# Optimization experiments

Measured on AMD Instinct MI355X. Metric: run time of the kernel, lower is better.

## Reference

```python
import jax, jax.numpy as jnp
import numpy as np

B, C, H, W = 16, 512, 32, 32
HW = H * W  # == input_features == output_features for shapes to be consistent


def setup_inputs() -> dict:
    key = jax.random.key(0)
    k1, k2, k3 = jax.random.split(key, 3)
    node1 = jax.random.normal(k1, (B, C, H, W), dtype=jnp.float32)
    node2 = jax.random.normal(k2, (B, C, H, W), dtype=jnp.float32)
    # nn.Linear(input_features, output_features, bias=False).weight: [out, in]
    W_c = jax.random.normal(k3, (HW, HW), dtype=jnp.float32) * (1.0 / np.sqrt(HW))
    return {"node1": node1, "node2": node2, "W_c": W_c}


def reference(node1, node2, W_c):
    b, c, h, w = node1.shape
    hw = h * w
    n1 = node1.reshape(b, c, hw)  # [B, C, HW]
    n2 = node2.reshape(b, c, hw)  # [B, C, HW]
    # x = W_c(n1): Linear applies y = x @ W^T  -> [B, C, HW_out]
    x = jnp.einsum('bch,oh->bco', n1, W_c)
    # e = bmm(x.permute(0,2,1), n2): [B, HW_out, C] @ [B, C, HW] -> [B, HW_out, HW]
    e = jnp.einsum('bco,bch->boh', x, n2)
    a = jax.nn.softmax(e, axis=-1)  # softmax over last dim (HW of node2)
    # m = bmm(n2, a): [B, C, HW] @ [B, HW, HW] -> [B, C, HW]
    m = jnp.einsum('bck,bkj->bcj', n2, a)
    return m
```

## Files before the change

kernel.cpp:

```cpp
#include <hip/hip_runtime.h>
#include <math.h>


typedef _Float16 f16;
typedef _Float16 f16x8 __attribute__((ext_vector_type(8)));
typedef _Float16 f16x4 __attribute__((ext_vector_type(4)));
typedef float f32x4 __attribute__((ext_vector_type(4)));

#define WG_BARRIER() asm volatile("s_waitcnt lgkmcnt(0)\ns_barrier" ::: "memory")

__global__ __launch_bounds__(256) void prep(const float* __restrict__ n1,
                                            const float* __restrict__ Wc,
                                            const float* __restrict__ n2,
                                            f16* __restrict__ n1f, f16* __restrict__ Wf,
                                            f16* __restrict__ n2f, f16* __restrict__ n2t) {
    const int bid = blockIdx.x, tid = threadIdx.x;
    if (bid < 4608) {
        const float* s = (bid < 4096) ? n1 : Wc;
        f16* d = (bid < 4096) ? n1f : Wf;
        const size_t i = ((size_t)(bid < 4096 ? bid : bid - 4096) * 256 + tid) * 8;
        f32x4 a = *(const f32x4*)(s + i);
        f32x4 b = *(const f32x4*)(s + i + 4);
        f16x8 o;
        o[0] = (f16)a[0]; o[1] = (f16)a[1]; o[2] = (f16)a[2]; o[3] = (f16)a[3];
        o[4] = (f16)b[0]; o[5] = (f16)b[1]; o[6] = (f16)b[2]; o[7] = (f16)b[3];
        *(f16x8*)(d + i) = o;
        return;
    }
    const int id = bid - 4608;
    const int b = id >> 7;
    const int ry = (id & 127) >> 4;
    const int cx = id & 15;
    const float* S = n2 + (size_t)b * 512 * 1024;
    f16* Dn = n2f + (size_t)b * 512 * 1024;
    f16* Dt = n2t + (size_t)b * 1024 * 512;
    __shared__ f16 Ts[64 * 72];
    const int r0 = ry * 64, c0 = cx * 64;
    const int rr = tid >> 3, cc8 = (tid & 7) * 8;
#pragma unroll
    for (int h = 0; h < 2; ++h) {
        const int row = r0 + rr + 32 * h;
        const float* s = S + (size_t)row * 1024 + c0 + cc8;
        f32x4 a = *(const f32x4*)s, bq = *(const f32x4*)(s + 4);
        f16x8 o;
        o[0] = (f16)a[0]; o[1] = (f16)a[1]; o[2] = (f16)a[2]; o[3] = (f16)a[3];
        o[4] = (f16)bq[0]; o[5] = (f16)bq[1]; o[6] = (f16)bq[2]; o[7] = (f16)bq[3];
        *(f16x8*)&Ts[(rr + 32 * h) * 72 + cc8] = o;
        *(f16x8*)(Dn + (size_t)row * 1024 + c0 + cc8) = o;
    }
    __syncthreads();
    const int j = tid >> 2, k16 = (tid & 3) * 16;
    f16* d = Dt + (size_t)(c0 + j) * 512 + r0 + k16;
    f16x8 o0, o1;
#pragma unroll
    for (int i = 0; i < 8; ++i) {
        o0[i] = Ts[(k16 + i) * 72 + j];
        o1[i] = Ts[(k16 + 8 + i) * 72 + j];
    }
    *(f16x8*)d = o0;
    *(f16x8*)(d + 8) = o1;
}

__global__ __launch_bounds__(256) void softmax_stats(const f16* __restrict__ E,
                                                     float* __restrict__ Mg,
                                                     float* __restrict__ Si) {
    const int wave = threadIdx.x >> 6, lane = threadIdx.x & 63;
    const int row = blockIdx.x * 4 + wave;
    const f16* p = E + (size_t)row * 1024 + lane * 16;
    f16x8 a = *(const f16x8*)p, b = *(const f16x8*)(p + 8);
    float v[16];
#pragma unroll
    for (int i = 0; i < 8; ++i) { v[i] = (float)a[i]; v[i + 8] = (float)b[i]; }
    float m = v[0];
#pragma unroll
    for (int i = 1; i < 16; ++i) m = fmaxf(m, v[i]);
#pragma unroll
    for (int off = 1; off < 64; off <<= 1) m = fmaxf(m, __shfl_xor(m, off, 64));
    float s = 0.f;
#pragma unroll
    for (int i = 0; i < 16; ++i) s += __expf(v[i] - m);
#pragma unroll
    for (int off = 1; off < 64; off <<= 1) s += __shfl_xor(s, off, 64);
    if (lane == 0) { Mg[row] = m; Si[row] = 1.0f / s; }
}

__global__ __launch_bounds__(256) void tr_scale(const f16* __restrict__ S,
                                                const float* __restrict__ Mg,
                                                const float* __restrict__ Si,
                                                f16* __restrict__ D) {
    const int b = blockIdx.z;
    S += (size_t)b * 1024 * 1024;
    D += (size_t)b * 1024 * 1024;
    __shared__ f16 Ts[64 * 72];
    const int r0 = blockIdx.y * 64, c0 = blockIdx.x * 64;
    const int tid = threadIdx.x;
    const int rr = tid >> 3, cc8 = (tid & 7) * 8;
#pragma unroll
    for (int h = 0; h < 2; ++h) {
        const int row = r0 + rr + 32 * h;
        const float mg = Mg[b * 1024 + row];
        const float si = Si[b * 1024 + row];
        f16x8 v = *(const f16x8*)(S + (size_t)row * 1024 + c0 + cc8);
        f16x8 o;
#pragma unroll
        for (int i = 0; i < 8; ++i) o[i] = (f16)(__expf((float)v[i] - mg) * si);
        *(f16x8*)&Ts[(rr + 32 * h) * 72 + cc8] = o;
    }
    __syncthreads();
    const int j = tid >> 2, k16 = (tid & 3) * 16;
    f16* d = D + (size_t)(c0 + j) * 1024 + r0 + k16;
    f16x8 o0, o1;
#pragma unroll
    for (int i = 0; i < 8; ++i) {
        o0[i] = Ts[(k16 + i) * 72 + j];
        o1[i] = Ts[(k16 + 8 + i) * 72 + j];
    }
    *(f16x8*)d = o0;
    *(f16x8*)(d + 8) = o1;
}

#define GEMM_CORE(NS)                                                                   \
    f16x8 ra = *(const f16x8*)gAp, rb = *(const f16x8*)gBp;                             \
    *(f16x8*)wA0 = ra; *(f16x8*)wB0 = rb;                                               \
    ra = *(const f16x8*)(gAp + 64); rb = *(const f16x8*)(gBp + 64);                     \
    WG_BARRIER();                                                                       \
    f32x4 acc[4][2] = {};                                                               \
_Pragma("unroll")                                                                       \
    for (int kb = 0; kb < (NS); ++kb) {                                                 \
        const f16* Ac = (const f16*)(SM + (kb & 1) * 8192);                             \
        const f16* Bc = (const f16*)(SM + 16384 + (kb & 1) * 8192);                     \
        f16x8 fa[4], fb[2];                                                             \
_Pragma("unroll")                                                                       \
        for (int u = 0; u < 4; ++u)                                                     \
            fa[u] = *(const f16x8*)&Ac[(wm + u * 16 + col) * 32 + quad * 8];            \
_Pragma("unroll")                                                                       \
        for (int v = 0; v < 2; ++v)                                                     \
            fb[v] = *(const f16x8*)&Bc[(wn + v * 16 + col) * 32 + quad * 8];            \
_Pragma("unroll")                                                                       \
        for (int u = 0; u < 4; ++u)                                                     \
_Pragma("unroll")                                                                       \
            for (int v = 0; v < 2; ++v)                                                 \
                acc[u][v] = __builtin_amdgcn_mfma_f32_16x16x32_f16(fa[u], fb[v],        \
                                                                   acc[u][v], 0, 0, 0);\
        if (kb + 1 < (NS)) {                                                            \
            char* dA = SM + ((kb + 1) & 1) * 8192 + off;                                \
            char* dB = SM + 16384 + ((kb + 1) & 1) * 8192 + off;                        \
            *(f16x8*)dA = ra;                                                           \
            *(f16x8*)dB = rb;                                                           \
            if (kb + 2 < (NS)) {                                                        \
                ra = *(const f16x8*)(gAp + (size_t)(kb + 2) * 64);                      \
                rb = *(const f16x8*)(gBp + (size_t)(kb + 2) * 64);                      \
            }                                                                           \
            WG_BARRIER();                                                               \
        }                                                                               \
    }

__global__ __launch_bounds__(512) void gemm1_nt_xt(const f16* __restrict__ A,
                                                   const f16* __restrict__ Bw,
                                                   f16* __restrict__ Xt) {
    const int M = 512, K = 1024;
    const int id = blockIdx.x;
    const int xcd = id & 7, loc = id >> 3;
    const int b = xcd * 2 + (loc >> 5);
    const int m0 = ((loc >> 3) & 3) * 128;
    const int n0 = (loc & 7) * 128;
    A += (size_t)b * M * K;
    Xt += (size_t)b * 1024 * M;
    __shared__ __attribute__((aligned(16))) char SM[34816];
    const int tid = threadIdx.x, lane = tid & 63, wave = tid >> 6;
    const int col = lane & 15, quad = lane >> 4;
    const int wm = (wave & 1) * 64, wn = (wave >> 1) * 32;
    const int off = wave * 1024 + lane * 16;
    const int srow = off >> 6, scolb = off & 63;
    const char* gAp = (const char*)A + (size_t)(m0 + srow) * K * 2 + scolb;
    const char* gBp = (const char*)Bw + (size_t)(n0 + srow) * K * 2 + scolb;
    char* wA0 = SM + off;
    char* wB0 = SM + 16384 + off;

    GEMM_CORE(32)

    WG_BARRIER();
    f16* Tt = (f16*)SM;
#pragma unroll
    for (int u = 0; u < 4; ++u)
#pragma unroll
        for (int v = 0; v < 2; ++v) {
            f16x4 p;
#pragma unroll
            for (int r = 0; r < 4; ++r) p[r] = (f16)acc[u][v][r];
            *(f16x4*)&Tt[(wn + v * 16 + col) * 136 + wm + u * 16 + quad * 4] = p;
        }
    WG_BARRIER();
    const int j = tid >> 2, seg = (tid & 3) * 32;
    f16* dst = Xt + (size_t)(n0 + j) * M + m0 + seg;
#pragma unroll
    for (int c8 = 0; c8 < 32; c8 += 8)
        *(f16x8*)(dst + c8) = *(const f16x8*)&Tt[j * 136 + seg + c8];
}

__global__ __launch_bounds__(512) void gemm2_nt_e(const f16* __restrict__ A,
                                                  const f16* __restrict__ B,
                                                  f16* __restrict__ E) {
    const int K = 512;
    const int id = blockIdx.x;
    const int xcd = id & 7, loc = id >> 3;
    const int b = xcd * 2 + (loc >> 6);
    const int m0 = ((loc >> 3) & 7) * 128;
    const int n0 = (loc & 7) * 128;
    A += (size_t)b * 1024 * K;
    B += (size_t)b * 1024 * K;
    E += (size_t)b * 1024 * 1024;
    __shared__ __attribute__((aligned(16))) char SM[32768];
    const int tid = threadIdx.x, lane = tid & 63, wave = tid >> 6;
    const int col = lane & 15, quad = lane >> 4;
    const int wm = (wave & 1) * 64, wn = (wave >> 1) * 32;
    const int off = wave * 1024 + lane * 16;
    const int srow = off >> 6, scolb = off & 63;
    const char* gAp = (const char*)A + (size_t)(m0 + srow) * K * 2 + scolb;
    const char* gBp = (const char*)B + (size_t)(n0 + srow) * K * 2 + scolb;
    char* wA0 = SM + off;
    char* wB0 = SM + 16384 + off;

    GEMM_CORE(16)

#pragma unroll
    for (int u = 0; u < 4; ++u)
#pragma unroll
        for (int v = 0; v < 2; ++v)
#pragma unroll
            for (int r = 0; r < 4; ++r)
                E[(size_t)(m0 + wm + u * 16 + quad * 4 + r) * 1024 + n0 + wn + v * 16 + col] =
                    (f16)acc[u][v][r];
}

__global__ __launch_bounds__(512) void gemm3_nt_out(const f16* __restrict__ A,
                                                    const f16* __restrict__ Bt,
                                                    float* __restrict__ C) {
    const int K = 1024;
    const int id = blockIdx.x;
    const int xcd = id & 7, loc = id >> 3;
    const int b = xcd * 2 + (loc >> 5);
    const int m0 = ((loc >> 3) & 3) * 128;
    const int n0 = (loc & 7) * 128;
    A += (size_t)b * 512 * K;
    Bt += (size_t)b * 1024 * K;
    C += (size_t)b * 512 * 1024;
    __shared__ __attribute__((aligned(16))) char SM[32768];
    const int tid = threadIdx.x, lane = tid & 63, wave = tid >> 6;
    const int col = lane & 15, quad = lane >> 4;
    const int wm = (wave & 1) * 64, wn = (wave >> 1) * 32;
    const int off = wave * 1024 + lane * 16;
    const int srow = off >> 6, scolb = off & 63;
    const char* gAp = (const char*)A + (size_t)(m0 + srow) * K * 2 + scolb;
    const char* gBp = (const char*)Bt + (size_t)(n0 + srow) * K * 2 + scolb;
    char* wA0 = SM + off;
    char* wB0 = SM + 16384 + off;

    GEMM_CORE(32)

#pragma unroll
    for (int u = 0; u < 4; ++u)
#pragma unroll
        for (int v = 0; v < 2; ++v)
#pragma unroll
            for (int r = 0; r < 4; ++r)
                C[(size_t)(m0 + wm + u * 16 + quad * 4 + r) * 1024 + n0 + wn + v * 16 + col] =
                    acc[u][v][r];
}

extern "C" void kernel_launch(void* const* d_in, const int* in_sizes, int n_in,
                              void* d_out, int out_size, void* d_ws, size_t ws_size,
                              hipStream_t stream) {
    const float* n1 = (const float*)d_in[0];
    const float* n2 = (const float*)d_in[1];
    const float* Wc = (const float*)d_in[2];
    float* out = (float*)d_out;
    char* ws = (char*)d_ws;

    f16* n2t = (f16*)(ws);
    f16* Xt  = (f16*)(ws + (16u << 20));
    f16* Wf  = (f16*)(ws + (32u << 20));
    f16* E   = (f16*)(ws + (32u << 20));
    f16* n1f = (f16*)(ws + (64u << 20));
    f16* n2f = (f16*)(ws + (80u << 20));
    float* Mg = (float*)(ws + (64u << 20));
    float* Si = (float*)(ws + (64u << 20) + (1u << 16));
    f16* At  = (f16*)(ws);

    prep<<<6656, dim3(256), 0, stream>>>(n1, Wc, n2, n1f, Wf, n2f, n2t);
    gemm1_nt_xt<<<512, dim3(512), 0, stream>>>(n1f, Wf, Xt);
    gemm2_nt_e<<<1024, dim3(512), 0, stream>>>(Xt, n2t, E);
    softmax_stats<<<4096, dim3(256), 0, stream>>>(E, Mg, Si);
    tr_scale<<<dim3(16, 16, 16), dim3(256), 0, stream>>>(E, Mg, Si, At);
    gemm3_nt_out<<<512, dim3(512), 0, stream>>>(n2f, At, out);
}
```

Baseline: 205.4 us.

## Write transposed scores, compute column logsumexp, fuse softmax exp into final GEMM

gemm2 now writes the score matrix already transposed through an LDS staging tile. Softmax statistics are computed as per-column online max/sum partials and then combined into a log-sum-exp per row. The separate transpose-and-scale pass is removed: gemm3 applies exp(e - lse) while staging the B tile into shared memory. The GEMM core also gains a second register prefetch stage (depth-2). This saves a full read and write of the 16x1024x1024 half-precision attention matrix, in exchange for more exp work inside the GEMM loop and a partial-statistics pass with strided loads.

```diff
diff --git a/kernel.cpp b/kernel.cpp
--- a/kernel.cpp
+++ b/kernel.cpp
@@ -61,68 +61,53 @@
     *(f16x8*)(d + 8) = o1;
 }
 
-__global__ __launch_bounds__(256) void softmax_stats(const f16* __restrict__ E,
-                                                     float* __restrict__ Mg,
-                                                     float* __restrict__ Si) {
-    const int wave = threadIdx.x >> 6, lane = threadIdx.x & 63;
-    const int row = blockIdx.x * 4 + wave;
-    const f16* p = E + (size_t)row * 1024 + lane * 16;
-    f16x8 a = *(const f16x8*)p, b = *(const f16x8*)(p + 8);
-    float v[16];
-#pragma unroll
-    for (int i = 0; i < 8; ++i) { v[i] = (float)a[i]; v[i + 8] = (float)b[i]; }
-    float m = v[0];
-#pragma unroll
-    for (int i = 1; i < 16; ++i) m = fmaxf(m, v[i]);
-#pragma unroll
-    for (int off = 1; off < 64; off <<= 1) m = fmaxf(m, __shfl_xor(m, off, 64));
-    float s = 0.f;
-#pragma unroll
-    for (int i = 0; i < 16; ++i) s += __expf(v[i] - m);
-#pragma unroll
-    for (int off = 1; off < 64; off <<= 1) s += __shfl_xor(s, off, 64);
-    if (lane == 0) { Mg[row] = m; Si[row] = 1.0f / s; }
-}
-
-__global__ __launch_bounds__(256) void tr_scale(const f16* __restrict__ S,
-                                                const float* __restrict__ Mg,
-                                                const float* __restrict__ Si,
-                                                f16* __restrict__ D) {
-    const int b = blockIdx.z;
-    S += (size_t)b * 1024 * 1024;
-    D += (size_t)b * 1024 * 1024;
-    __shared__ f16 Ts[64 * 72];
-    const int r0 = blockIdx.y * 64, c0 = blockIdx.x * 64;
-    const int tid = threadIdx.x;
-    const int rr = tid >> 3, cc8 = (tid & 7) * 8;
-#pragma unroll
-    for (int h = 0; h < 2; ++h) {
-        const int row = r0 + rr + 32 * h;
-        const float mg = Mg[b * 1024 + row];
-        const float si = Si[b * 1024 + row];
-        f16x8 v = *(const f16x8*)(S + (size_t)row * 1024 + c0 + cc8);
-        f16x8 o;
-#pragma unroll
-        for (int i = 0; i < 8; ++i) o[i] = (f16)(__expf((float)v[i] - mg) * si);
-        *(f16x8*)&Ts[(rr + 32 * h) * 72 + cc8] = o;
-    }
-    __syncthreads();
-    const int j = tid >> 2, k16 = (tid & 3) * 16;
-    f16* d = D + (size_t)(c0 + j) * 1024 + r0 + k16;
-    f16x8 o0, o1;
-#pragma unroll
-    for (int i = 0; i < 8; ++i) {
-        o0[i] = Ts[(k16 + i) * 72 + j];
-        o1[i] = Ts[(k16 + 8 + i) * 72 + j];
-    }
-    *(f16x8*)d = o0;
-    *(f16x8*)(d + 8) = o1;
-}
-
-#define GEMM_CORE(NS)                                                                   \
-    f16x8 ra = *(const f16x8*)gAp, rb = *(const f16x8*)gBp;                             \
-    *(f16x8*)wA0 = ra; *(f16x8*)wB0 = rb;                                               \
-    ra = *(const f16x8*)(gAp + 64); rb = *(const f16x8*)(gBp + 64);                     \
+__global__ __launch_bounds__(256) void stats_partial(const f16* __restrict__ Et,
+                                                     float* __restrict__ Pm,
+                                                     float* __restrict__ Ps) {
+    const int b = blockIdx.x & 15, chunk = blockIdx.x >> 4;
+    const int t = threadIdx.x;
+    const f16* p = Et + (size_t)b * 1024 * 1024 + (size_t)chunk * 64 * 1024 + t * 4;
+    float m[4] = {-3.0e38f, -3.0e38f, -3.0e38f, -3.0e38f};
+    float s[4] = {0.f, 0.f, 0.f, 0.f};
+#pragma unroll 4
+    for (int j = 0; j < 64; ++j) {
+        f16x4 v4 = *(const f16x4*)(p + (size_t)j * 1024);
+#pragma unroll
+        for (int c = 0; c < 4; ++c) {
+            float v = (float)v4[c];
+            float nm = fmaxf(m[c], v);
+            s[c] = s[c] * __expf(m[c] - nm) + __expf(v - nm);
+            m[c] = nm;
+        }
+    }
+    f32x4 mo, so;
+#pragma unroll
+    for (int c = 0; c < 4; ++c) { mo[c] = m[c]; so[c] = s[c]; }
+    *(f32x4*)(Pm + (size_t)(b * 16 + chunk) * 1024 + t * 4) = mo;
+    *(f32x4*)(Ps + (size_t)(b * 16 + chunk) * 1024 + t * 4) = so;
+}
+
+__global__ __launch_bounds__(256) void stats_combine(const float* __restrict__ Pm,
+                                                     const float* __restrict__ Ps,
+                                                     float* __restrict__ Sc) {
+    const int g = blockIdx.x * 256 + threadIdx.x;
+    const int b = g >> 10, o = g & 1023;
+    const float* pm = Pm + (size_t)b * 16 * 1024 + o;
+    const float* ps = Ps + (size_t)b * 16 * 1024 + o;
+    float M = -3.0e38f;
+#pragma unroll
+    for (int c = 0; c < 16; ++c) M = fmaxf(M, pm[c * 1024]);
+    float S = 0.f;
+#pragma unroll
+    for (int c = 0; c < 16; ++c) S += ps[c * 1024] * __expf(pm[c * 1024] - M);
+    Sc[g] = M + __logf(S);
+}
+
+#define GEMM_CORE_D2(NS)                                                                \
+    f16x8 pa0 = *(const f16x8*)gAp, pb0 = *(const f16x8*)gBp;                           \
+    *(f16x8*)wA0 = pa0; *(f16x8*)wB0 = pb0;                                             \
+    f16x8 pa1 = *(const f16x8*)(gAp + 64), pb1 = *(const f16x8*)(gBp + 64);             \
+    pa0 = *(const f16x8*)(gAp + 128); pb0 = *(const f16x8*)(gBp + 128);                 \
     WG_BARRIER();                                                                       \
     f32x4 acc[4][2] = {};                                                               \
 _Pragma("unroll")                                                                       \
@@ -145,11 +130,18 @@
         if (kb + 1 < (NS)) {                                                            \
             char* dA = SM + ((kb + 1) & 1) * 8192 + off;                                \
             char* dB = SM + 16384 + ((kb + 1) & 1) * 8192 + off;                        \
-            *(f16x8*)dA = ra;                                                           \
-            *(f16x8*)dB = rb;                                                           \
-            if (kb + 2 < (NS)) {                                                        \
-                ra = *(const f16x8*)(gAp + (size_t)(kb + 2) * 64);                      \
-                rb = *(const f16x8*)(gBp + (size_t)(kb + 2) * 64);                      \
+            if ((kb & 1) == 0) {                                                        \
+                *(f16x8*)dA = pa1; *(f16x8*)dB = pb1;                                   \
+                if (kb + 3 < (NS)) {                                                    \
+                    pa1 = *(const f16x8*)(gAp + (size_t)(kb + 3) * 64);                 \
+                    pb1 = *(const f16x8*)(gBp + (size_t)(kb + 3) * 64);                 \
+                }                                                                       \
+            } else {                                                                    \
+                *(f16x8*)dA = pa0; *(f16x8*)dB = pb0;                                   \
+                if (kb + 3 < (NS)) {                                                    \
+                    pa0 = *(const f16x8*)(gAp + (size_t)(kb + 3) * 64);                 \
+                    pb0 = *(const f16x8*)(gBp + (size_t)(kb + 3) * 64);                 \
+                }                                                                       \
             }                                                                           \
             WG_BARRIER();                                                               \
         }                                                                               \
@@ -177,7 +169,7 @@
     char* wA0 = SM + off;
     char* wB0 = SM + 16384 + off;
 
-    GEMM_CORE(32)
+    GEMM_CORE_D2(32)
 
     WG_BARRIER();
     f16* Tt = (f16*)SM;
@@ -198,9 +190,9 @@
         *(f16x8*)(dst + c8) = *(const f16x8*)&Tt[j * 136 + seg + c8];
 }
 
-__global__ __launch_bounds__(512) void gemm2_nt_e(const f16* __restrict__ A,
-                                                  const f16* __restrict__ B,
-                                                  f16* __restrict__ E) {
+__global__ __launch_bounds__(512) void gemm2_nt_et(const f16* __restrict__ A,
+                                                   const f16* __restrict__ B,
+                                                   f16* __restrict__ Et) {
     const int K = 512;
     const int id = blockIdx.x;
     const int xcd = id & 7, loc = id >> 3;
@@ -209,8 +201,8 @@
     const int n0 = (loc & 7) * 128;
     A += (size_t)b * 1024 * K;
     B += (size_t)b * 1024 * K;
-    E += (size_t)b * 1024 * 1024;
-    __shared__ __attribute__((aligned(16))) char SM[32768];
+    Et += (size_t)b * 1024 * 1024;
+    __shared__ __attribute__((aligned(16))) char SM[34816];
     const int tid = threadIdx.x, lane = tid & 63, wave = tid >> 6;
     const int col = lane & 15, quad = lane >> 4;
     const int wm = (wave & 1) * 64, wn = (wave >> 1) * 32;
@@ -221,29 +213,40 @@
     char* wA0 = SM + off;
     char* wB0 = SM + 16384 + off;
 
-    GEMM_CORE(16)
-
+    GEMM_CORE_D2(16)
+
+    WG_BARRIER();
+    f16* Tt = (f16*)SM;
 #pragma unroll
     for (int u = 0; u < 4; ++u)
 #pragma unroll
-        for (int v = 0; v < 2; ++v)
-#pragma unroll
-            for (int r = 0; r < 4; ++r)
-                E[(size_t)(m0 + wm + u * 16 + quad * 4 + r) * 1024 + n0 + wn + v * 16 + col] =
-                    (f16)acc[u][v][r];
+        for (int v = 0; v < 2; ++v) {
+            f16x4 p;
+#pragma unroll
+            for (int r = 0; r < 4; ++r) p[r] = (f16)acc[u][v][r];
+            *(f16x4*)&Tt[(wn + v * 16 + col) * 136 + wm + u * 16 + quad * 4] = p;
+        }
+    WG_BARRIER();
+    const int j = tid >> 2, seg = (tid & 3) * 32;
+    f16* dst = Et + (size_t)(n0 + j) * 1024 + m0 + seg;
+#pragma unroll
+    for (int c8 = 0; c8 < 32; c8 += 8)
+        *(f16x8*)(dst + c8) = *(const f16x8*)&Tt[j * 136 + seg + c8];
 }
 
 __global__ __launch_bounds__(512) void gemm3_nt_out(const f16* __restrict__ A,
-                                                    const f16* __restrict__ Bt,
+                                                    const f16* __restrict__ Et,
+                                                    const float* __restrict__ Sc,
                                                     float* __restrict__ C) {
-    const int K = 1024;
+    const int K = 1024, NS = 32;
     const int id = blockIdx.x;
     const int xcd = id & 7, loc = id >> 3;
     const int b = xcd * 2 + (loc >> 5);
     const int m0 = ((loc >> 3) & 3) * 128;
     const int n0 = (loc & 7) * 128;
     A += (size_t)b * 512 * K;
-    Bt += (size_t)b * 1024 * K;
+    Et += (size_t)b * 1024 * K;
+    Sc += (size_t)b * 1024;
     C += (size_t)b * 512 * 1024;
     __shared__ __attribute__((aligned(16))) char SM[32768];
     const int tid = threadIdx.x, lane = tid & 63, wave = tid >> 6;
@@ -252,11 +255,64 @@
     const int off = wave * 1024 + lane * 16;
     const int srow = off >> 6, scolb = off & 63;
     const char* gAp = (const char*)A + (size_t)(m0 + srow) * K * 2 + scolb;
-    const char* gBp = (const char*)Bt + (size_t)(n0 + srow) * K * 2 + scolb;
+    const char* gBp = (const char*)Et + (size_t)(n0 + srow) * K * 2 + scolb;
+    const float* gSp = Sc + (scolb >> 1);
     char* wA0 = SM + off;
     char* wB0 = SM + 16384 + off;
 
-    GEMM_CORE(32)
+    f16x8 ra = *(const f16x8*)gAp, rb = *(const f16x8*)gBp;
+    f32x4 c0 = *(const f32x4*)gSp, c1 = *(const f32x4*)(gSp + 4);
+    {
+        f16x8 rbs;
+#pragma unroll
+        for (int i = 0; i < 4; ++i) rbs[i] = (f16)__expf((float)rb[i] - c0[i]);
+#pragma unroll
+        for (int i = 0; i < 4; ++i) rbs[4 + i] = (f16)__expf((float)rb[4 + i] - c1[i]);
+        *(f16x8*)wA0 = ra;
+        *(f16x8*)wB0 = rbs;
+    }
+    ra = *(const f16x8*)(gAp + 64);
+    rb = *(const f16x8*)(gBp + 64);
+    c0 = *(const f32x4*)(gSp + 32);
+    c1 = *(const f32x4*)(gSp + 36);
+    WG_BARRIER();
+    f32x4 acc[4][2] = {};
+#pragma unroll
+    for (int kb = 0; kb < NS; ++kb) {
+        const f16* Ac = (const f16*)(SM + (kb & 1) * 8192);
+        const f16* Bc = (const f16*)(SM + 16384 + (kb & 1) * 8192);
+        f16x8 fa[4], fb[2];
+#pragma unroll
+        for (int u = 0; u < 4; ++u)
+            fa[u] = *(const f16x8*)&Ac[(wm + u * 16 + col) * 32 + quad * 8];
+#pragma unroll
+        for (int v = 0; v < 2; ++v)
+            fb[v] = *(const f16x8*)&Bc[(wn + v * 16 + col) * 32 + quad * 8];
+#pragma unroll
+        for (int u = 0; u < 4; ++u)
+#pragma unroll
+            for (int v = 0; v < 2; ++v)
+                acc[u][v] = __builtin_amdgcn_mfma_f32_16x16x32_f16(fa[u], fb[v],
+                                                                   acc[u][v], 0, 0, 0);
+        if (kb + 1 < NS) {
+            char* dA = SM + ((kb + 1) & 1) * 8192 + off;
+            char* dB = SM + 16384 + ((kb + 1) & 1) * 8192 + off;
+            f16x8 rbs;
+#pragma unroll
+            for (int i = 0; i < 4; ++i) rbs[i] = (f16)__expf((float)rb[i] - c0[i]);
+#pragma unroll
+            for (int i = 0; i < 4; ++i) rbs[4 + i] = (f16)__expf((float)rb[4 + i] - c1[i]);
+            *(f16x8*)dA = ra;
+            *(f16x8*)dB = rbs;
+            if (kb + 2 < NS) {
+                ra = *(const f16x8*)(gAp + (size_t)(kb + 2) * 64);
+                rb = *(const f16x8*)(gBp + (size_t)(kb + 2) * 64);
+                c0 = *(const f32x4*)(gSp + (size_t)(kb + 2) * 32);
+                c1 = *(const f32x4*)(gSp + (size_t)(kb + 2) * 32 + 4);
+            }
+            WG_BARRIER();
+        }
+    }
 
 #pragma unroll
     for (int u = 0; u < 4; ++u)
@@ -280,17 +336,17 @@
     f16* n2t = (f16*)(ws);
     f16* Xt  = (f16*)(ws + (16u << 20));
     f16* Wf  = (f16*)(ws + (32u << 20));
-    f16* E   = (f16*)(ws + (32u << 20));
+    f16* Et  = (f16*)(ws + (32u << 20));
     f16* n1f = (f16*)(ws + (64u << 20));
     f16* n2f = (f16*)(ws + (80u << 20));
-    float* Mg = (float*)(ws + (64u << 20));
-    float* Si = (float*)(ws + (64u << 20) + (1u << 16));
-    f16* At  = (f16*)(ws);
+    float* Pm = (float*)(ws + (64u << 20));
+    float* Ps = (float*)(ws + (65u << 20));
+    float* Sc = (float*)(ws + (66u << 20));
 
     prep<<<6656, dim3(256), 0, stream>>>(n1, Wc, n2, n1f, Wf, n2f, n2t);
     gemm1_nt_xt<<<512, dim3(512), 0, stream>>>(n1f, Wf, Xt);
-    gemm2_nt_e<<<1024, dim3(512), 0, stream>>>(Xt, n2t, E);
-    softmax_stats<<<4096, dim3(256), 0, stream>>>(E, Mg, Si);
-    tr_scale<<<dim3(16, 16, 16), dim3(256), 0, stream>>>(E, Mg, Si, At);
-    gemm3_nt_out<<<512, dim3(512), 0, stream>>>(n2f, At, out);
-}
+    gemm2_nt_et<<<1024, dim3(512), 0, stream>>>(Xt, n2t, Et);
+    stats_partial<<<256, dim3(256), 0, stream>>>(Et, Pm, Ps);
+    stats_combine<<<64, dim3(256), 0, stream>>>(Pm, Ps, Sc);
+    gemm3_nt_out<<<512, dim3(512), 0, stream>>>(n2f, Et, Sc, out);
+}
```

Result: slower. 210.0 us (+2.2%).
